# Kernel optimization log

Measured on AMD Instinct MI355X. Metric: run time of the kernel, lower is better.

The kernel has to match this reference:

```python
import jax, jax.numpy as jnp
import numpy as np

N_HEAD = 16
NEG_INF = jnp.float32(-1e30)


def setup_inputs() -> dict:
    key = jax.random.key(0)
    k1, k2, k3 = jax.random.split(key, 3)
    B, T, C = 2, 2048, 1024
    x = jax.random.normal(k1, (B, T, C), dtype=jnp.float32)
    attn_mask = jnp.ones((B, T), dtype=jnp.int32)
    W_qkv = jax.random.normal(k2, (C, 3 * C), dtype=jnp.float32) * (1.0 / np.sqrt(C))
    b_qkv = jnp.zeros((3 * C,), dtype=jnp.float32)
    W_proj = jax.random.normal(k3, (C, C), dtype=jnp.float32) * (1.0 / np.sqrt(C))
    b_proj = jnp.zeros((C,), dtype=jnp.float32)
    return {"x": x, "attn_mask": attn_mask, "W_qkv": W_qkv, "b_qkv": b_qkv,
            "W_proj": W_proj, "b_proj": b_proj}


def reference(x, attn_mask, W_qkv, b_qkv, W_proj, b_proj):
    B, T, C = x.shape
    H = N_HEAD
    hd = C // H
    qkv = x @ W_qkv + b_qkv                       # [B,T,3C]
    q, k, v = jnp.split(qkv, 3, axis=-1)
    q = q.reshape(B, T, H, hd).transpose(0, 2, 1, 3)  # [B,H,T,hd]
    k = k.reshape(B, T, H, hd).transpose(0, 2, 1, 3)
    v = v.reshape(B, T, H, hd).transpose(0, 2, 1, 3)
    att = jnp.einsum('bhqd,bhkd->bhqk', q, k) / jnp.float32(np.sqrt(hd))  # [B,H,T,T]
    causal = jnp.tril(jnp.ones((T, T), dtype=bool))[None, None]           # [1,1,T,T]
    pad = (attn_mask != 0)[:, None, None, :]                              # [B,1,1,T]
    att = jnp.where(causal & pad, att, NEG_INF)
    att = jax.nn.softmax(att, axis=-1)
    y = jnp.einsum('bhqk,bhkd->bhqd', att, v)     # [B,H,T,hd]
    y = y.transpose(0, 2, 1, 3).reshape(B, T, C)
    return y @ W_proj + b_proj
```

## Files before the change

kernel.cpp:

```cpp
#include <hip/hip_runtime.h>

#define T_SEQ 2048
#define NHEAD 16
#define HD 64
#define CDIM 1024

typedef __bf16 bf16x8 __attribute__((ext_vector_type(8)));
typedef float f32x4 __attribute__((ext_vector_type(4)));

union U16x8 { uint4 u4; unsigned short s[8]; bf16x8 b; };

__device__ __forceinline__ float bf2f(unsigned short u) {
    return __uint_as_float(((unsigned int)u) << 16);
}
__device__ __forceinline__ unsigned short f2bf(float f) {
    unsigned int u = __float_as_uint(f);
    u += 0x7fffu + ((u >> 16) & 1u);
    return (unsigned short)(u >> 16);
}
__device__ __forceinline__ unsigned short f2bf_fast(float f) {
    return (unsigned short)((__float_as_uint(f) + 0x8000u) >> 16);
}
__device__ __forceinline__ U16x8 load8f(const float* __restrict__ p) {
    U16x8 r;
    float4 f0 = *(const float4*)p;
    float4 f1 = *(const float4*)(p + 4);
    r.s[0] = f2bf(f0.x); r.s[1] = f2bf(f0.y); r.s[2] = f2bf(f0.z); r.s[3] = f2bf(f0.w);
    r.s[4] = f2bf(f1.x); r.s[5] = f2bf(f1.y); r.s[6] = f2bf(f1.z); r.s[7] = f2bf(f1.w);
    return r;
}

__device__ __forceinline__ void async_copy16(const unsigned short* g, unsigned short* l) {
    __builtin_amdgcn_global_load_lds(
        (const __attribute__((address_space(1))) unsigned int*)g,
        (__attribute__((address_space(3))) unsigned int*)l, 16, 0, 0);
}

#define LOG2E 1.442695040f

__global__ __launch_bounds__(256) void conv_bf16(
    const float* __restrict__ in, unsigned short* __restrict__ out, int n)
{
    const int i = (blockIdx.x * 256 + threadIdx.x) * 8;
    if (i < n) {
        U16x8 o = load8f(&in[i]);
        *(uint4*)&out[i] = o.u4;
    }
}

__global__ __launch_bounds__(256) void transpose_conv(
    const float* __restrict__ in, unsigned short* __restrict__ out, int R, int C)
{
    __shared__ float tile[64][65];
    const int r0 = blockIdx.x * 64;
    const int c0 = blockIdx.y * 64;
    const int tid = threadIdx.x;
    const int rr = tid >> 4;
    const int cc = (tid & 15) * 4;
#pragma unroll
    for (int p = 0; p < 4; ++p) {
        float4 v = *(const float4*)&in[(size_t)(r0 + p * 16 + rr) * C + c0 + cc];
        tile[p * 16 + rr][cc] = v.x;
        tile[p * 16 + rr][cc + 1] = v.y;
        tile[p * 16 + rr][cc + 2] = v.z;
        tile[p * 16 + rr][cc + 3] = v.w;
    }
    __syncthreads();
    const int n = tid >> 2;
    const int s = (tid & 3) * 8;
#pragma unroll
    for (int p = 0; p < 2; ++p) {
        const int k = s + p * 32;
        U16x8 o;
#pragma unroll
        for (int j = 0; j < 8; ++j) o.s[j] = f2bf(tile[k + j][n]);
        *(uint4*)&out[(size_t)(c0 + n) * R + r0 + k] = o.u4;
    }
}

__device__ __forceinline__ void gemm128_core(
    const unsigned short* __restrict__ A,
    const unsigned short* __restrict__ Bt,
    int K, int m0, int n0,
    unsigned short* As, unsigned short* Bs, f32x4 acc[4][4])
{
    const int tid = threadIdx.x;
    const int w = tid >> 6, lane = tid & 63;
    const int ln = lane & 15, quad = lane >> 4;
    const int wm = w >> 1, wn = w & 1;
    const int lr = lane >> 3;
    const int lc = (lane & 7) * 8;

    for (int kb = 0; kb < K; kb += 64) {
        __syncthreads();
#pragma unroll
        for (int i = 0; i < 4; ++i) {
            async_copy16(&A[(size_t)(m0 + w * 32 + i * 8 + lr) * K + kb + lc],
                         &As[(w * 32 + i * 8) * 64]);
            async_copy16(&Bt[(size_t)(n0 + w * 32 + i * 8 + lr) * K + kb + lc],
                         &Bs[(w * 32 + i * 8) * 64]);
        }
        __syncthreads();
#pragma unroll
        for (int kk = 0; kk < 2; ++kk) {
            U16x8 af[4], bff[4];
#pragma unroll
            for (int i = 0; i < 4; ++i)
                af[i].u4 = *(const uint4*)&As[(wm * 64 + i * 16 + ln) * 64 + kk * 32 + quad * 8];
#pragma unroll
            for (int j = 0; j < 4; ++j)
                bff[j].u4 = *(const uint4*)&Bs[(wn * 64 + j * 16 + ln) * 64 + kk * 32 + quad * 8];
#pragma unroll
            for (int i = 0; i < 4; ++i)
#pragma unroll
                for (int j = 0; j < 4; ++j)
                    acc[i][j] = __builtin_amdgcn_mfma_f32_16x16x32_bf16(af[i].b, bff[j].b, acc[i][j], 0, 0, 0);
        }
    }
}

__global__ __launch_bounds__(256) void qkv_fused(
    const unsigned short* __restrict__ Xb,
    const unsigned short* __restrict__ Wt,
    const float* __restrict__ bias,
    unsigned short* __restrict__ Qp,
    unsigned short* __restrict__ Kp,
    unsigned short* __restrict__ Vtp)
{
    __shared__ unsigned short As[128 * 64];
    __shared__ unsigned short Bs[128 * 64];

    const int bid = blockIdx.x;
    const int tid = threadIdx.x;
    const int w = tid >> 6, lane = tid & 63;
    const int ln = lane & 15, quad = lane >> 4;
    const int wm = w >> 1, wn = w & 1;

    f32x4 acc[4][4];
#pragma unroll
    for (int i = 0; i < 4; ++i)
#pragma unroll
        for (int j = 0; j < 4; ++j) acc[i][j] = (f32x4){0.f, 0.f, 0.f, 0.f};

    if (bid < 512) {
        const int n0 = (bid & 15) * 128;
        const int m0 = (bid >> 4) * 128;
        gemm128_core(Xb, Wt, CDIM, m0, n0, As, Bs, acc);

#pragma unroll
        for (int j = 0; j < 4; ++j) {
            const int n = n0 + wn * 64 + j * 16 + ln;
            const float bv = bias[n];
            const int which = n >> 10;
            const int h = (n >> 6) & 15, d = n & 63;
            unsigned short* dst = which == 0 ? Qp : Kp;
#pragma unroll
            for (int i = 0; i < 4; ++i)
#pragma unroll
                for (int r = 0; r < 4; ++r) {
                    const int m = m0 + wm * 64 + i * 16 + quad * 4 + r;
                    const int b = m >> 11, tt = m & 2047;
                    dst[(((b * NHEAD + h) * T_SEQ) + tt) * HD + d] = f2bf(acc[i][j][r] + bv);
                }
        }
    } else {
        const int u = bid - 512;
        const int n0 = (u & 31) * 128;
        const int m0 = (u >> 5) * 128;
        const unsigned short* WvT = Wt + (size_t)2048 * CDIM;
        gemm128_core(WvT, Xb, CDIM, m0, n0, As, Bs, acc);

#pragma unroll
        for (int i = 0; i < 4; ++i)
#pragma unroll
            for (int r = 0; r < 4; ++r) {
                const int row = m0 + wm * 64 + i * 16 + quad * 4 + r;
                const float bv = bias[2048 + row];
#pragma unroll
                for (int j = 0; j < 4; ++j) {
                    const int n = n0 + wn * 64 + j * 16 + ln;
                    const int b = n >> 11, tt = n & 2047;
                    Vtp[(size_t)(b * 1024 + row) * T_SEQ + tt] = f2bf(acc[i][j][r] + bv);
                }
            }
    }
}

__global__ __launch_bounds__(256) void proj_gemm(
    const unsigned short* __restrict__ Yin,
    const unsigned short* __restrict__ Wt,
    const float* __restrict__ bias,
    float* __restrict__ out)
{
    __shared__ unsigned short As[128 * 64];
    __shared__ unsigned short Bs[128 * 64];
    const int m0 = blockIdx.y * 128;
    const int n0 = blockIdx.x * 128;

    f32x4 acc[4][4];
#pragma unroll
    for (int i = 0; i < 4; ++i)
#pragma unroll
        for (int j = 0; j < 4; ++j) acc[i][j] = (f32x4){0.f, 0.f, 0.f, 0.f};

    gemm128_core(Yin, Wt, CDIM, m0, n0, As, Bs, acc);

    const int tid = threadIdx.x;
    const int w = tid >> 6, lane = tid & 63;
    const int ln = lane & 15, quad = lane >> 4;
    const int wm = w >> 1, wn = w & 1;

#pragma unroll
    for (int j = 0; j < 4; ++j) {
        const int n = n0 + wn * 64 + j * 16 + ln;
        const float bv = bias[n];
#pragma unroll
        for (int i = 0; i < 4; ++i)
#pragma unroll
            for (int r = 0; r < 4; ++r) {
                const int m = m0 + wm * 64 + i * 16 + quad * 4 + r;
                out[(size_t)m * CDIM + n] = acc[i][j][r] + bv;
            }
    }
}

#define ATT_STRIDE 72

__global__ __launch_bounds__(256) void flash_attn(
    const unsigned short* __restrict__ Qp,
    const unsigned short* __restrict__ Kp,
    const unsigned short* __restrict__ Vtp,
    const int* __restrict__ mask,
    unsigned short* __restrict__ Y)
{
    __shared__ unsigned short Ks[64 * ATT_STRIDE];
    __shared__ unsigned short Vs[64 * ATT_STRIDE];
    __shared__ unsigned short Ps[64 * ATT_STRIDE];
    __shared__ float mask_f[64];

    const int bh = blockIdx.x;
    const int qt = (T_SEQ / 64 - 1) - blockIdx.y;
    const int b = bh >> 4, h = bh & 15;
    const int tid = threadIdx.x;
    const int w = tid >> 6, lane = tid & 63;
    const int ln = lane & 15, quad = lane >> 4;
    const int row8 = tid >> 3, seg = tid & 7;
    const size_t base = (size_t)bh * T_SEQ * HD;
    const int q0 = qt * 64;

    U16x8 qf[2];
    {
        const unsigned short* qrow = &Qp[base + (size_t)(q0 + w * 16 + ln) * HD];
        qf[0].u4 = *(const uint4*)&qrow[quad * 8];
        qf[1].u4 = *(const uint4*)&qrow[32 + quad * 8];
    }

    f32x4 o[4];
#pragma unroll
    for (int n = 0; n < 4; ++n) o[n] = (f32x4){0.f, 0.f, 0.f, 0.f};
    float m_i[4] = {-3.0e38f, -3.0e38f, -3.0e38f, -3.0e38f};
    float l_i[4] = {0.f, 0.f, 0.f, 0.f};

    uint4 kr0, kr1, vr0, vr1;
    float mf = 0.f;
    {
        const unsigned short* kp0 = &Kp[base + (size_t)row8 * HD + seg * 8];
        kr0 = *(const uint4*)kp0;
        kr1 = *(const uint4*)(kp0 + 32 * HD);
        const unsigned short* vp0 = &Vtp[base + (size_t)row8 * T_SEQ + seg * 8];
        vr0 = *(const uint4*)vp0;
        vr1 = *(const uint4*)(vp0 + 32 * T_SEQ);
        if (tid < 64) mf = mask[b * T_SEQ + tid] ? 0.f : -1.0e30f;
    }

    for (int j = 0; j <= qt; ++j) {
        __syncthreads();
        *(uint4*)&Ks[row8 * ATT_STRIDE + seg * 8] = kr0;
        *(uint4*)&Ks[(row8 + 32) * ATT_STRIDE + seg * 8] = kr1;
        *(uint4*)&Vs[row8 * ATT_STRIDE + seg * 8] = vr0;
        *(uint4*)&Vs[(row8 + 32) * ATT_STRIDE + seg * 8] = vr1;
        if (tid < 64) mask_f[tid] = mf;
        __syncthreads();

        if (j < qt) {
            const unsigned short* kp0 = &Kp[base + (size_t)((j + 1) * 64 + row8) * HD + seg * 8];
            kr0 = *(const uint4*)kp0;
            kr1 = *(const uint4*)(kp0 + 32 * HD);
            const unsigned short* vp0 = &Vtp[base + (size_t)row8 * T_SEQ + (j + 1) * 64 + seg * 8];
            vr0 = *(const uint4*)vp0;
            vr1 = *(const uint4*)(vp0 + 32 * T_SEQ);
            if (tid < 64) mf = mask[b * T_SEQ + (j + 1) * 64 + tid] ? 0.f : -1.0e30f;
        }

        const bool diag = (j == qt);

        f32x4 sc[4];
#pragma unroll
        for (int t = 0; t < 4; ++t) sc[t] = (f32x4){0.f, 0.f, 0.f, 0.f};
#pragma unroll
        for (int t = 0; t < 4; ++t) {
            if (diag && t > w) continue;
#pragma unroll
            for (int s = 0; s < 2; ++s) {
                U16x8 kb;
                kb.u4 = *(const uint4*)&Ks[(t * 16 + ln) * ATT_STRIDE + s * 32 + quad * 8];
                sc[t] = __builtin_amdgcn_mfma_f32_16x16x32_bf16(qf[s].b, kb.b, sc[t], 0, 0, 0);
            }
        }

        float rm[4] = {-3.0e38f, -3.0e38f, -3.0e38f, -3.0e38f};
#pragma unroll
        for (int t = 0; t < 4; ++t) {
            if (diag && t > w) {
#pragma unroll
                for (int i = 0; i < 4; ++i) sc[t][i] = -1.0e30f;
            } else {
                const float madd = mask_f[t * 16 + ln];
                const bool edge = diag && (t == w);
#pragma unroll
                for (int i = 0; i < 4; ++i) {
                    float v = fmaf(sc[t][i], 0.125f, madd);
                    if (edge && ln > quad * 4 + i) v = -1.0e30f;
                    sc[t][i] = v;
                    rm[i] = fmaxf(rm[i], v);
                }
            }
        }
#pragma unroll
        for (int i = 0; i < 4; ++i) {
            rm[i] = fmaxf(rm[i], __shfl_xor(rm[i], 1));
            rm[i] = fmaxf(rm[i], __shfl_xor(rm[i], 2));
            rm[i] = fmaxf(rm[i], __shfl_xor(rm[i], 4));
            rm[i] = fmaxf(rm[i], __shfl_xor(rm[i], 8));
        }

        float alpha[4], mlog[4];
#pragma unroll
        for (int i = 0; i < 4; ++i) {
            const float nm = fmaxf(m_i[i], rm[i]);
            alpha[i] = __builtin_amdgcn_exp2f((m_i[i] - nm) * LOG2E);
            m_i[i] = nm;
            mlog[i] = nm * LOG2E;
        }
        float rsp[4] = {0.f, 0.f, 0.f, 0.f};
#pragma unroll
        for (int t = 0; t < 4; ++t)
#pragma unroll
            for (int i = 0; i < 4; ++i) {
                const float p = __builtin_amdgcn_exp2f(fmaf(sc[t][i], LOG2E, -mlog[i]));
                sc[t][i] = p;
                rsp[i] += p;
            }
#pragma unroll
        for (int i = 0; i < 4; ++i) l_i[i] = l_i[i] * alpha[i] + rsp[i];
#pragma unroll
        for (int n = 0; n < 4; ++n)
#pragma unroll
            for (int i = 0; i < 4; ++i) o[n][i] *= alpha[i];

#pragma unroll
        for (int t = 0; t < 4; ++t)
#pragma unroll
            for (int i = 0; i < 4; ++i)
                Ps[(w * 16 + quad * 4 + i) * ATT_STRIDE + t * 16 + ln] = f2bf_fast(sc[t][i]);

        U16x8 pa[2];
        pa[0].u4 = *(const uint4*)&Ps[(w * 16 + ln) * ATT_STRIDE + quad * 8];
        pa[1].u4 = *(const uint4*)&Ps[(w * 16 + ln) * ATT_STRIDE + 32 + quad * 8];

#pragma unroll
        for (int n = 0; n < 4; ++n)
#pragma unroll
            for (int s = 0; s < 2; ++s) {
                U16x8 vb;
                vb.u4 = *(const uint4*)&Vs[(n * 16 + ln) * ATT_STRIDE + s * 32 + quad * 8];
                o[n] = __builtin_amdgcn_mfma_f32_16x16x32_bf16(pa[s].b, vb.b, o[n], 0, 0, 0);
            }
    }

#pragma unroll
    for (int i = 0; i < 4; ++i) {
        float l = l_i[i];
        l += __shfl_xor(l, 1);
        l += __shfl_xor(l, 2);
        l += __shfl_xor(l, 4);
        l += __shfl_xor(l, 8);
        const float inv = 1.0f / l;
        const size_t row = (size_t)(b * T_SEQ + q0 + w * 16 + quad * 4 + i);
#pragma unroll
        for (int n = 0; n < 4; ++n)
            Y[row * CDIM + h * HD + n * 16 + ln] = f2bf(o[n][i] * inv);
    }
}

extern "C" void kernel_launch(void* const* d_in, const int* in_sizes, int n_in,
                              void* d_out, int out_size, void* d_ws, size_t ws_size,
                              hipStream_t stream)
{
    const float* X     = (const float*)d_in[0];
    const int*   mask  = (const int*)d_in[1];
    const float* Wqkv  = (const float*)d_in[2];
    const float* bqkv  = (const float*)d_in[3];
    const float* Wproj = (const float*)d_in[4];
    const float* bproj = (const float*)d_in[5];
    float* out = (float*)d_out;

    const size_t per = (size_t)2 * NHEAD * T_SEQ * HD;
    unsigned short* Qp     = (unsigned short*)d_ws;
    unsigned short* Kp     = Qp + per;
    unsigned short* Vtp    = Kp + per;
    unsigned short* Xb     = Vtp + per;
    unsigned short* Yp     = Xb;
    unsigned short* Wqkvt  = Xb + per;
    unsigned short* Wprojt = Wqkvt + (size_t)3 * CDIM * CDIM;

    conv_bf16<<<2048, 256, 0, stream>>>(X, Xb, 4 * 1024 * 1024);
    transpose_conv<<<dim3(16, 48), 256, 0, stream>>>(Wqkv, Wqkvt, CDIM, 3 * CDIM);
    transpose_conv<<<dim3(16, 16), 256, 0, stream>>>(Wproj, Wprojt, CDIM, CDIM);

    qkv_fused<<<768, 256, 0, stream>>>(Xb, Wqkvt, bqkv, Qp, Kp, Vtp);
    flash_attn<<<dim3(2 * NHEAD, T_SEQ / 64), 256, 0, stream>>>(Qp, Kp, Vtp, mask, Yp);
    proj_gemm<<<dim3(8, 32), 256, 0, stream>>>(Yp, Wprojt, bproj, out);
}
```

Before: 218.4 us.

## Replace QKV GEMM with 256x256 tile, 8-wave, double-buffered async pipeline

Rewrites the QKV projection GEMM to use 256x256 output tiles with 512 threads. Tiles are staged via async global-to-LDS copies into double buffers with an XOR swizzle, interleaved with MFMA quarters under explicit barriers, waitcnts and setprio. It also swizzles block order for L2 reuse and stores V with packed 4-element writes instead of scalar transposed writes. The goal is to raise MFMA utilization and cut global/LDS traffic per FLOP. The risks are 192 blocks underfilling 256 CUs and a fragile hand-written wait schedule.

```diff
diff --git a/kernel.cpp b/kernel.cpp
--- a/kernel.cpp
+++ b/kernel.cpp
@@ -38,6 +38,11 @@
 
 #define LOG2E 1.442695040f
 
+#define BAR()    asm volatile("s_barrier" ::: "memory")
+#define LGKM0()  asm volatile("s_waitcnt lgkmcnt(0)" ::: "memory")
+#define VMC6()   asm volatile("s_waitcnt vmcnt(6)" ::: "memory")
+#define VMC0()   asm volatile("s_waitcnt vmcnt(0)" ::: "memory")
+
 __global__ __launch_bounds__(256) void conv_bf16(
     const float* __restrict__ in, unsigned short* __restrict__ out, int n)
 {
@@ -119,7 +124,83 @@
     }
 }
 
-__global__ __launch_bounds__(256) void qkv_fused(
+
+__device__ __forceinline__ void stageA(const unsigned short* __restrict__ A,
+                                       unsigned short* buf,
+                                       int m0, int t, int unit, int w, int lane)
+{
+#pragma unroll
+    for (int s = 0; s < 2; ++s) {
+        const int r0 = s * 128 + unit * 64 + w * 8;
+        const int row = r0 + (lane >> 3);
+        const int col = (16 * (lane & 7)) ^ ((row & 4) ? 32 : 0);
+        const unsigned short* src = A + (size_t)(m0 + row) * CDIM + t * 64 + (col >> 1);
+        async_copy16(src, buf + r0 * 64);
+    }
+}
+
+__device__ __forceinline__ void stageB(const unsigned short* __restrict__ B,
+                                       unsigned short* buf,
+                                       int n0, int t, int unit, int w, int lane)
+{
+#pragma unroll
+    for (int s = 0; s < 2; ++s) {
+        const int slice = s * 8 + w;
+        const int r0 = (slice >> 2) * 64 + unit * 32 + (slice & 3) * 8;
+        const int row = r0 + (lane >> 3);
+        const int col = (16 * (lane & 7)) ^ ((row & 4) ? 32 : 0);
+        const unsigned short* src = B + (size_t)(n0 + row) * CDIM + t * 64 + (col >> 1);
+        async_copy16(src, buf + r0 * 64);
+    }
+}
+
+__device__ __forceinline__ void readA(U16x8 af[4][2], const unsigned short* buf,
+                                      int wm, int qm, int ln, int quad)
+{
+#pragma unroll
+    for (int i = 0; i < 4; ++i) {
+        const int row = wm * 128 + qm * 64 + i * 16 + ln;
+        const int sw = (row & 4) ? 32 : 0;
+#pragma unroll
+        for (int kk = 0; kk < 2; ++kk) {
+            const int byt = row * 128 + ((kk * 64 + quad * 16) ^ sw);
+            af[i][kk].u4 = *(const uint4*)((const char*)buf + byt);
+        }
+    }
+}
+
+__device__ __forceinline__ void readB(U16x8 bf[2][2], const unsigned short* buf,
+                                      int wn, int qn, int ln, int quad)
+{
+#pragma unroll
+    for (int jj = 0; jj < 2; ++jj) {
+        const int row = wn * 64 + qn * 32 + jj * 16 + ln;
+        const int sw = (row & 4) ? 32 : 0;
+#pragma unroll
+        for (int kk = 0; kk < 2; ++kk) {
+            const int byt = row * 128 + ((kk * 64 + quad * 16) ^ sw);
+            bf[jj][kk].u4 = *(const uint4*)((const char*)buf + byt);
+        }
+    }
+}
+
+template<int QM, int QN>
+__device__ __forceinline__ void mfma16(f32x4 acc[8][4], const U16x8 af[4][2],
+                                       const U16x8 bf[2][2])
+{
+    __builtin_amdgcn_s_setprio(1);
+#pragma unroll
+    for (int i = 0; i < 4; ++i)
+#pragma unroll
+        for (int jj = 0; jj < 2; ++jj)
+#pragma unroll
+            for (int kk = 0; kk < 2; ++kk)
+                acc[QM * 4 + i][QN * 2 + jj] = __builtin_amdgcn_mfma_f32_16x16x32_bf16(
+                    af[i][kk].b, bf[jj][kk].b, acc[QM * 4 + i][QN * 2 + jj], 0, 0, 0);
+    __builtin_amdgcn_s_setprio(0);
+}
+
+__global__ __launch_bounds__(512) void qkv8(
     const unsigned short* __restrict__ Xb,
     const unsigned short* __restrict__ Wt,
     const float* __restrict__ bias,
@@ -127,62 +208,143 @@
     unsigned short* __restrict__ Kp,
     unsigned short* __restrict__ Vtp)
 {
-    __shared__ unsigned short As[128 * 64];
-    __shared__ unsigned short Bs[128 * 64];
-
-    const int bid = blockIdx.x;
+    __shared__ __align__(1024) unsigned short smem[4][16384];
+    unsigned short* Ab0 = smem[0];
+    unsigned short* Ab1 = smem[1];
+    unsigned short* Bb0 = smem[2];
+    unsigned short* Bb1 = smem[3];
+
     const int tid = threadIdx.x;
     const int w = tid >> 6, lane = tid & 63;
     const int ln = lane & 15, quad = lane >> 4;
-    const int wm = w >> 1, wn = w & 1;
-
-    f32x4 acc[4][4];
-#pragma unroll
-    for (int i = 0; i < 4; ++i)
+    const int wm = w >> 2, wn = w & 3;
+
+    const int bid = blockIdx.x;
+    const int swz = (bid & 7) * 24 + (bid >> 3);
+    const int nt = swz % 12, mt = swz / 12;
+    const int m0 = mt * 256, n0 = nt * 256;
+
+    f32x4 acc[8][4];
+#pragma unroll
+    for (int i = 0; i < 8; ++i)
 #pragma unroll
         for (int j = 0; j < 4; ++j) acc[i][j] = (f32x4){0.f, 0.f, 0.f, 0.f};
 
-    if (bid < 512) {
-        const int n0 = (bid & 15) * 128;
-        const int m0 = (bid >> 4) * 128;
-        gemm128_core(Xb, Wt, CDIM, m0, n0, As, Bs, acc);
-
-#pragma unroll
-        for (int j = 0; j < 4; ++j) {
-            const int n = n0 + wn * 64 + j * 16 + ln;
-            const float bv = bias[n];
-            const int which = n >> 10;
+    stageA(Xb, Ab0, m0, 0, 0, w, lane);
+    stageB(Wt, Bb0, n0, 0, 0, w, lane);
+    stageB(Wt, Bb0, n0, 0, 1, w, lane);
+    stageA(Xb, Ab0, m0, 0, 1, w, lane);
+    stageA(Xb, Ab1, m0, 1, 0, w, lane);
+    stageB(Wt, Bb1, n0, 1, 0, w, lane);
+    stageB(Wt, Bb1, n0, 1, 1, w, lane);
+    VMC6();
+    BAR();
+
+    U16x8 af[4][2], bq0[2][2], bq1[2][2];
+
+    for (int j = 0; j < 7; ++j) {
+        const int e = 2 * j, o = 2 * j + 1;
+        readA(af, Ab0, wm, 0, ln, quad);
+        readB(bq0, Bb0, wn, 0, ln, quad);
+        stageA(Xb, Ab1, m0, o, 1, w, lane);
+        BAR(); LGKM0();
+        mfma16<0, 0>(acc, af, bq0);
+        LGKM0(); BAR();
+        readB(bq1, Bb0, wn, 1, ln, quad);
+        stageA(Xb, Ab0, m0, e + 2, 0, w, lane);
+        BAR(); LGKM0();
+        mfma16<0, 1>(acc, af, bq1);
+        LGKM0(); BAR();
+        readA(af, Ab0, wm, 1, ln, quad);
+        stageB(Wt, Bb0, n0, e + 2, 0, w, lane);
+        BAR(); LGKM0();
+        mfma16<1, 0>(acc, af, bq0);
+        LGKM0(); BAR();
+        stageB(Wt, Bb0, n0, e + 2, 1, w, lane);
+        BAR();
+        mfma16<1, 1>(acc, af, bq1);
+        VMC6(); BAR();
+        readA(af, Ab1, wm, 0, ln, quad);
+        readB(bq0, Bb1, wn, 0, ln, quad);
+        stageA(Xb, Ab0, m0, e + 2, 1, w, lane);
+        BAR(); LGKM0();
+        mfma16<0, 0>(acc, af, bq0);
+        LGKM0(); BAR();
+        readB(bq1, Bb1, wn, 1, ln, quad);
+        stageA(Xb, Ab1, m0, o + 2, 0, w, lane);
+        BAR(); LGKM0();
+        mfma16<0, 1>(acc, af, bq1);
+        LGKM0(); BAR();
+        readA(af, Ab1, wm, 1, ln, quad);
+        stageB(Wt, Bb1, n0, o + 2, 0, w, lane);
+        BAR(); LGKM0();
+        mfma16<1, 0>(acc, af, bq0);
+        LGKM0(); BAR();
+        stageB(Wt, Bb1, n0, o + 2, 1, w, lane);
+        BAR();
+        mfma16<1, 1>(acc, af, bq1);
+        VMC6(); BAR();
+    }
+
+    stageA(Xb, Ab1, m0, 15, 1, w, lane);
+    VMC0(); BAR();
+
+    readA(af, Ab0, wm, 0, ln, quad);
+    readB(bq0, Bb0, wn, 0, ln, quad);
+    readB(bq1, Bb0, wn, 1, ln, quad);
+    mfma16<0, 0>(acc, af, bq0);
+    mfma16<0, 1>(acc, af, bq1);
+    readA(af, Ab0, wm, 1, ln, quad);
+    mfma16<1, 0>(acc, af, bq0);
+    mfma16<1, 1>(acc, af, bq1);
+
+    readA(af, Ab1, wm, 0, ln, quad);
+    readB(bq0, Bb1, wn, 0, ln, quad);
+    readB(bq1, Bb1, wn, 1, ln, quad);
+    mfma16<0, 0>(acc, af, bq0);
+    mfma16<0, 1>(acc, af, bq1);
+    readA(af, Ab1, wm, 1, ln, quad);
+    mfma16<1, 0>(acc, af, bq0);
+    mfma16<1, 1>(acc, af, bq1);
+
+    const int which = n0 >> 10;
+    float bv[4];
+#pragma unroll
+    for (int jj = 0; jj < 4; ++jj) bv[jj] = bias[n0 + wn * 64 + jj * 16 + ln];
+
+    if (which < 2) {
+        unsigned short* dst = (which == 0) ? Qp : Kp;
+#pragma unroll
+        for (int jj = 0; jj < 4; ++jj) {
+            const int n = n0 + wn * 64 + jj * 16 + ln;
             const int h = (n >> 6) & 15, d = n & 63;
-            unsigned short* dst = which == 0 ? Qp : Kp;
-#pragma unroll
-            for (int i = 0; i < 4; ++i)
+#pragma unroll
+            for (int i = 0; i < 8; ++i)
 #pragma unroll
                 for (int r = 0; r < 4; ++r) {
-                    const int m = m0 + wm * 64 + i * 16 + quad * 4 + r;
+                    const int m = m0 + wm * 128 + i * 16 + quad * 4 + r;
                     const int b = m >> 11, tt = m & 2047;
-                    dst[(((b * NHEAD + h) * T_SEQ) + tt) * HD + d] = f2bf(acc[i][j][r] + bv);
+                    dst[(((size_t)(b * NHEAD + h) * T_SEQ) + tt) * HD + d] =
+                        f2bf(acc[i][jj][r] + bv[jj]);
                 }
         }
     } else {
-        const int u = bid - 512;
-        const int n0 = (u & 31) * 128;
-        const int m0 = (u >> 5) * 128;
-        const unsigned short* WvT = Wt + (size_t)2048 * CDIM;
-        gemm128_core(WvT, Xb, CDIM, m0, n0, As, Bs, acc);
-
-#pragma unroll
-        for (int i = 0; i < 4; ++i)
-#pragma unroll
-            for (int r = 0; r < 4; ++r) {
-                const int row = m0 + wm * 64 + i * 16 + quad * 4 + r;
-                const float bv = bias[2048 + row];
-#pragma unroll
-                for (int j = 0; j < 4; ++j) {
-                    const int n = n0 + wn * 64 + j * 16 + ln;
-                    const int b = n >> 11, tt = n & 2047;
-                    Vtp[(size_t)(b * 1024 + row) * T_SEQ + tt] = f2bf(acc[i][j][r] + bv);
-                }
+#pragma unroll
+        for (int jj = 0; jj < 4; ++jj) {
+            const int n = n0 + wn * 64 + jj * 16 + ln;
+            const int c = n - 2048;
+#pragma unroll
+            for (int i = 0; i < 8; ++i) {
+                const int m00 = m0 + wm * 128 + i * 16 + quad * 4;
+                const int b = m00 >> 11, tt = m00 & 2047;
+                ushort4 pk;
+                pk.x = f2bf(acc[i][jj][0] + bv[jj]);
+                pk.y = f2bf(acc[i][jj][1] + bv[jj]);
+                pk.z = f2bf(acc[i][jj][2] + bv[jj]);
+                pk.w = f2bf(acc[i][jj][3] + bv[jj]);
+                *(ushort4*)&Vtp[(size_t)(b * 1024 + c) * T_SEQ + tt] = pk;
             }
+        }
     }
 }
 
@@ -418,7 +580,7 @@
     transpose_conv<<<dim3(16, 48), 256, 0, stream>>>(Wqkv, Wqkvt, CDIM, 3 * CDIM);
     transpose_conv<<<dim3(16, 16), 256, 0, stream>>>(Wproj, Wprojt, CDIM, CDIM);
 
-    qkv_fused<<<768, 256, 0, stream>>>(Xb, Wqkvt, bqkv, Qp, Kp, Vtp);
+    qkv8<<<192, 512, 0, stream>>>(Xb, Wqkvt, bqkv, Qp, Kp, Vtp);
     flash_attn<<<dim3(2 * NHEAD, T_SEQ / 64), 256, 0, stream>>>(Qp, Kp, Vtp, mask, Yp);
     proj_gemm<<<dim3(8, 32), 256, 0, stream>>>(Yp, Wprojt, bproj, out);
 }
```

New measurement: 216.9 us. Within noise of the previous version (-0.7%).
